# Optimization experiments

Hardware: AMD Instinct MI355X
Metric: run time of the kernel (lower is better)

Reference implementation:

```python
import jax, jax.numpy as jnp
import numpy as np

EPS = 1e-06


def setup_inputs() -> dict:
    key = jax.random.key(0)
    k1, k2, k3 = jax.random.split(key, 3)
    B, H, L, D = 4, 32, 4096, 128
    Q = jax.random.normal(k1, (B, H, L, D), dtype=jnp.float32)
    KV = jax.random.normal(k2, (B * H, D, D), dtype=jnp.float32)
    Z = jax.random.normal(k3, (B * H, D, 1), dtype=jnp.float32)
    return {"Q": Q, "KV": KV, "Z": Z}


def reference(Q, KV, Z):
    B, H, L, D = Q.shape
    Qr = Q.reshape(B * H, L, D)
    Q_phi = jax.nn.elu(Qr) + 1.0                      # [BH, L, D]
    numerator = jnp.einsum('bld,bde->ble', Q_phi, KV)  # [BH, L, D]
    denominator = jnp.einsum('bld,bdo->blo', Q_phi, Z) + EPS  # [BH, L, 1]
    out = numerator / denominator
    return out.reshape(B, H, L, D)
```

## Files before the change

kernel.cpp:

```cpp
#include <hip/hip_runtime.h>


#define BH   128
#define LQ   4096
#define DD   128
#define TL   128
#define APAD 136
#define EPS  1e-6

typedef __attribute__((ext_vector_type(8))) short bf16x8;
typedef __attribute__((ext_vector_type(4))) float f32x4;

__device__ __forceinline__ unsigned short f2bf_rne(float f){
  unsigned u = __float_as_uint(f);
  u += 0x7FFFu + ((u >> 16) & 1u);
  return (unsigned short)(u >> 16);
}
__device__ __forceinline__ float bf2f(unsigned short h){
  return __uint_as_float(((unsigned)h) << 16);
}

__global__ __launch_bounds__(256) void prep_b(const float* __restrict__ KV,
                                              unsigned short* __restrict__ Bhi,
                                              unsigned short* __restrict__ Blo){
  int flat = blockIdx.x * 256 + threadIdx.x;
  int lane = flat & 63;
  int kk   = (flat >> 6) & 3;
  int n0   = (flat >> 8) & 7;
  int bh   = flat >> 11;
  int e  = n0 * 16 + (lane & 15);
  int kb = kk * 32 + (lane >> 4) * 8;
  const float* src = KV + (size_t)bh * DD * DD + (size_t)kb * DD + e;
  unsigned h[8], l[8];
  #pragma unroll
  for (int j = 0; j < 8; j++){
    float v = src[(size_t)j * DD];
    unsigned short hh = f2bf_rne(v);
    h[j] = hh;
    l[j] = f2bf_rne(v - bf2f(hh));
  }
  uint4 hv, lv;
  hv.x = h[0] | (h[1] << 16); hv.y = h[2] | (h[3] << 16);
  hv.z = h[4] | (h[5] << 16); hv.w = h[6] | (h[7] << 16);
  lv.x = l[0] | (l[1] << 16); lv.y = l[2] | (l[3] << 16);
  lv.z = l[4] | (l[5] << 16); lv.w = l[6] | (l[7] << 16);
  size_t o = (size_t)flat * 8;
  *(uint4*)(Bhi + o) = hv;
  *(uint4*)(Blo + o) = lv;
}

__global__ __launch_bounds__(256, 3) void kat_main(const float* __restrict__ Q,
                                                   const float* __restrict__ Z,
                                                   const unsigned short* __restrict__ Bhi,
                                                   const unsigned short* __restrict__ Blo,
                                                   float* __restrict__ Out){
  __shared__ unsigned short Ahi[TL * APAD];
  __shared__ double sden[TL];
  __shared__ float  srden[TL];
  __shared__ int    snf;
  __shared__ int    slist[TL];

  const int bh = blockIdx.x;
  const int lt = blockIdx.y;
  const int t  = threadIdx.x;
  const size_t qbase = ((size_t)bh * LQ + (size_t)lt * TL) * DD;

  if (t == 0) snf = 0;

  const int c4 = t & 31;
  const float4 z4 = *(const float4*)(Z + (size_t)bh * DD + c4 * 4);
  const double zz0 = z4.x, zz1 = z4.y, zz2 = z4.z, zz3 = z4.w;

  #pragma unroll 4
  for (int i = 0; i < 16; i++){
    int idx = t + 256 * i;
    int row = idx >> 5;
    const float4 q = *(const float4*)(Q + qbase + (size_t)row * DD + c4 * 4);
    float p0 = q.x > 0.f ? q.x + 1.f : expf(q.x);
    float p1 = q.y > 0.f ? q.y + 1.f : expf(q.y);
    float p2 = q.z > 0.f ? q.z + 1.f : expf(q.z);
    float p3 = q.w > 0.f ? q.w + 1.f : expf(q.w);
    unsigned h0 = f2bf_rne(p0), h1 = f2bf_rne(p1), h2 = f2bf_rne(p2), h3 = f2bf_rne(p3);
    uint2 pk; pk.x = h0 | (h1 << 16); pk.y = h2 | (h3 << 16);
    *(uint2*)&Ahi[row * APAD + c4 * 4] = pk;
    double part = (double)p0 * zz0 + (double)p1 * zz1 + (double)p2 * zz2 + (double)p3 * zz3;
    #pragma unroll
    for (int msk = 16; msk >= 1; msk >>= 1) part += __shfl_xor(part, msk, 64);
    if ((t & 31) == 0) sden[row] = part;
  }
  __syncthreads();

  if (t < TL){
    if (fabs(sden[t]) < 0.01){
      int p = atomicAdd(&snf, 1);
      slist[p] = t;
    }
  }
  __syncthreads();
  int nf = snf;
  if (nf > 0 && t < 64){
    for (int f = 0; f < nf; f++){
      int r = slist[f];
      const float* qr = Q + qbase + (size_t)r * DD;
      int d0 = t * 2;
      double s = 0.0;
      #pragma unroll
      for (int u = 0; u < 2; u++){
        float qv = qr[d0 + u];
        double qphi = (qv > 0.f) ? ((double)qv + 1.0) : exp((double)qv);
        s += qphi * (double)Z[(size_t)bh * DD + d0 + u];
      }
      #pragma unroll
      for (int msk = 32; msk >= 1; msk >>= 1) s += __shfl_xor(s, msk, 64);
      if (t == 0) sden[r] = s;
    }
  }
  __syncthreads();
  if (t < TL) srden[t] = (float)(1.0 / (sden[t] + EPS));
  __syncthreads();

  const int lane = t & 63;
  const int w    = t >> 6;
  const int m    = lane & 15;
  const int quad = lane >> 4;
  const int r0   = w * 32;

  bf16x8 afr[2][4];
  #pragma unroll
  for (int rg = 0; rg < 2; rg++)
    #pragma unroll
    for (int kk = 0; kk < 4; kk++)
      afr[rg][kk] = *(const bf16x8*)&Ahi[(r0 + rg * 16 + m) * APAD + kk * 32 + quad * 8];

  float rd[2][4];
  #pragma unroll
  for (int rg = 0; rg < 2; rg++)
    #pragma unroll
    for (int reg = 0; reg < 4; reg++)
      rd[rg][reg] = srden[r0 + rg * 16 + quad * 4 + reg];

  const size_t fb0 = ((size_t)bh * 8) * 4 * 512 + (size_t)lane * 8;
  #pragma unroll 1
  for (int n0 = 0; n0 < 8; n0++){
    size_t fb = fb0 + (size_t)n0 * 4 * 512;
    bf16x8 bhf[4], blf[4];
    #pragma unroll
    for (int kk = 0; kk < 4; kk++) bhf[kk] = *(const bf16x8*)(Bhi + fb + kk * 512);
    #pragma unroll
    for (int kk = 0; kk < 4; kk++) blf[kk] = *(const bf16x8*)(Blo + fb + kk * 512);
    #pragma unroll
    for (int rg = 0; rg < 2; rg++){
      f32x4 acc = {0.f, 0.f, 0.f, 0.f};
      #pragma unroll
      for (int kk = 0; kk < 4; kk++){
        acc = __builtin_amdgcn_mfma_f32_16x16x32_bf16(afr[rg][kk], bhf[kk], acc, 0, 0, 0);
        acc = __builtin_amdgcn_mfma_f32_16x16x32_bf16(afr[rg][kk], blf[kk], acc, 0, 0, 0);
      }
      float* op = Out + qbase + (size_t)(r0 + rg * 16 + quad * 4) * DD + n0 * 16 + m;
      #pragma unroll
      for (int reg = 0; reg < 4; reg++)
        op[(size_t)reg * DD] = acc[reg] * rd[rg][reg];
    }
  }
}

extern "C" void kernel_launch(void* const* d_in, const int* in_sizes, int n_in,
                              void* d_out, int out_size, void* d_ws, size_t ws_size,
                              hipStream_t stream){
  const float* Q  = (const float*)d_in[0];
  const float* KV = (const float*)d_in[1];
  const float* Z  = (const float*)d_in[2];
  unsigned short* Bhi = (unsigned short*)d_ws;
  unsigned short* Blo = Bhi + (size_t)BH * DD * DD;

  prep_b<<<1024, 256, 0, stream>>>(KV, Bhi, Blo);
  dim3 grid(BH, LQ / TL);
  kat_main<<<grid, 256, 0, stream>>>(Q, Z, Bhi, Blo, (float*)d_out);
}
```

Baseline: 520.5 us.

## Split MFMA work by output columns per wave, prefetch B, swizzle grid

Each wave now owns 32 output columns across all 128 rows instead of 32 rows across all columns. Its B fragments (hi and lo bf16 splits) are loaded once into registers before the denominator barrier, so the global B fetch overlaps the Q/elu phase rather than being reloaded inside the n-loop. The MFMA chains are split into independent accumulators for the hi and lo parts, which are summed at the end. The grid is flattened and remapped across 8 groups, likely to spread work over XCDs and improve KV locality in L2; the cost is higher register pressure from holding 16 B fragments per thread.

```diff
diff --git a/kernel.cpp b/kernel.cpp
--- a/kernel.cpp
+++ b/kernel.cpp
@@ -56,12 +56,14 @@
                                                    float* __restrict__ Out){
   __shared__ unsigned short Ahi[TL * APAD];
   __shared__ double sden[TL];
-  __shared__ float  srden[TL];
+  __shared__ __align__(16) float srden[TL];
   __shared__ int    snf;
   __shared__ int    slist[TL];
 
-  const int bh = blockIdx.x;
-  const int lt = blockIdx.y;
+  const int flat = blockIdx.x;
+  const int wg   = (flat & 7) * ((BH * (LQ / TL)) / 8) + (flat >> 3);
+  const int bh = wg >> 5;
+  const int lt = wg & 31;
   const int t  = threadIdx.x;
   const size_t qbase = ((size_t)bh * LQ + (size_t)lt * TL) * DD;
 
@@ -87,6 +89,22 @@
     #pragma unroll
     for (int msk = 16; msk >= 1; msk >>= 1) part += __shfl_xor(part, msk, 64);
     if ((t & 31) == 0) sden[row] = part;
+  }
+
+  const int lane = t & 63;
+  const int w    = t >> 6;
+  bf16x8 bhf[2][4], blf[2][4];
+  {
+    const size_t fb0 = (size_t)bh * (DD * DD) + (size_t)lane * 8;
+    #pragma unroll
+    for (int n = 0; n < 2; n++){
+      const size_t fb = fb0 + (size_t)(2 * w + n) * 2048;
+      #pragma unroll
+      for (int kk = 0; kk < 4; kk++){
+        bhf[n][kk] = *(const bf16x8*)(Bhi + fb + kk * 512);
+        blf[n][kk] = *(const bf16x8*)(Blo + fb + kk * 512);
+      }
+    }
   }
   __syncthreads();
 
@@ -119,47 +137,37 @@
   if (t < TL) srden[t] = (float)(1.0 / (sden[t] + EPS));
   __syncthreads();
 
-  const int lane = t & 63;
-  const int w    = t >> 6;
   const int m    = lane & 15;
   const int quad = lane >> 4;
-  const int r0   = w * 32;
 
-  bf16x8 afr[2][4];
-  #pragma unroll
-  for (int rg = 0; rg < 2; rg++)
+  #pragma unroll 2
+  for (int rg = 0; rg < 8; rg++){
+    bf16x8 afr[4];
     #pragma unroll
     for (int kk = 0; kk < 4; kk++)
-      afr[rg][kk] = *(const bf16x8*)&Ahi[(r0 + rg * 16 + m) * APAD + kk * 32 + quad * 8];
+      afr[kk] = *(const bf16x8*)&Ahi[(rg * 16 + m) * APAD + kk * 32 + quad * 8];
+    const f32x4 rdv = *(const f32x4*)&srden[rg * 16 + quad * 4];
 
-  float rd[2][4];
-  #pragma unroll
-  for (int rg = 0; rg < 2; rg++)
+    f32x4 acc[2][2];
     #pragma unroll
-    for (int reg = 0; reg < 4; reg++)
-      rd[rg][reg] = srden[r0 + rg * 16 + quad * 4 + reg];
-
-  const size_t fb0 = ((size_t)bh * 8) * 4 * 512 + (size_t)lane * 8;
-  #pragma unroll 1
-  for (int n0 = 0; n0 < 8; n0++){
-    size_t fb = fb0 + (size_t)n0 * 4 * 512;
-    bf16x8 bhf[4], blf[4];
+    for (int n = 0; n < 2; n++){
+      acc[n][0] = (f32x4){0.f, 0.f, 0.f, 0.f};
+      acc[n][1] = (f32x4){0.f, 0.f, 0.f, 0.f};
+    }
     #pragma unroll
-    for (int kk = 0; kk < 4; kk++) bhf[kk] = *(const bf16x8*)(Bhi + fb + kk * 512);
+    for (int kk = 0; kk < 4; kk++){
+      acc[0][0] = __builtin_amdgcn_mfma_f32_16x16x32_bf16(afr[kk], bhf[0][kk], acc[0][0], 0, 0, 0);
+      acc[1][0] = __builtin_amdgcn_mfma_f32_16x16x32_bf16(afr[kk], bhf[1][kk], acc[1][0], 0, 0, 0);
+      acc[0][1] = __builtin_amdgcn_mfma_f32_16x16x32_bf16(afr[kk], blf[0][kk], acc[0][1], 0, 0, 0);
+      acc[1][1] = __builtin_amdgcn_mfma_f32_16x16x32_bf16(afr[kk], blf[1][kk], acc[1][1], 0, 0, 0);
+    }
     #pragma unroll
-    for (int kk = 0; kk < 4; kk++) blf[kk] = *(const bf16x8*)(Blo + fb + kk * 512);
-    #pragma unroll
-    for (int rg = 0; rg < 2; rg++){
-      f32x4 acc = {0.f, 0.f, 0.f, 0.f};
-      #pragma unroll
-      for (int kk = 0; kk < 4; kk++){
-        acc = __builtin_amdgcn_mfma_f32_16x16x32_bf16(afr[rg][kk], bhf[kk], acc, 0, 0, 0);
-        acc = __builtin_amdgcn_mfma_f32_16x16x32_bf16(afr[rg][kk], blf[kk], acc, 0, 0, 0);
-      }
-      float* op = Out + qbase + (size_t)(r0 + rg * 16 + quad * 4) * DD + n0 * 16 + m;
+    for (int n = 0; n < 2; n++){
+      f32x4 s = acc[n][0] + acc[n][1];
+      float* op = Out + qbase + (size_t)(rg * 16 + quad * 4) * DD + (2 * w + n) * 16 + m;
       #pragma unroll
       for (int reg = 0; reg < 4; reg++)
-        op[(size_t)reg * DD] = acc[reg] * rd[rg][reg];
+        op[(size_t)reg * DD] = s[reg] * rdv[reg];
     }
   }
 }
@@ -174,6 +182,5 @@
   unsigned short* Blo = Bhi + (size_t)BH * DD * DD;
 
   prep_b<<<1024, 256, 0, stream>>>(KV, Bhi, Blo);
-  dim3 grid(BH, LQ / TL);
-  kat_main<<<grid, 256, 0, stream>>>(Q, Z, Bhi, Blo, (float*)d_out);
+  kat_main<<<dim3(BH * (LQ / TL)), 256, 0, stream>>>(Q, Z, Bhi, Blo, (float*)d_out);
 }
```

Result: faster. 465.9 us (-10.5%).
